# Optimization experiments

Hardware: AMD Instinct MI355X
Metric: run time of the kernel (lower is better)

The kernel has to match this reference:

```python
import jax, jax.numpy as jnp
import numpy as np

D = 256      # d_model
NH = 8       # heads
NL = 3       # layers
DFF = 1024   # ffn hidden
WIN = 64     # attention window
EPS = 1e-5


def _sin_pos_embed(L, d):
    # Sinusoidal positional embedding, matches _create_pos_embedding.
    pos = jnp.arange(L, dtype=jnp.float32)[:, None]
    div = jnp.exp(jnp.arange(0, d, 2, dtype=jnp.float32) * (-np.log(10000.0) / d))
    pe = jnp.zeros((L, d), jnp.float32)
    pe = pe.at[:, 0::2].set(jnp.sin(pos * div))
    pe = pe.at[:, 1::2].set(jnp.cos(pos * div))
    return pe  # [L, D]


def _layer_norm(x, scale, bias):
    m = jnp.mean(x, axis=-1, keepdims=True)
    v = jnp.mean(jnp.square(x - m), axis=-1, keepdims=True)
    return (x - m) * jax.lax.rsqrt(v + EPS) * scale + bias


def _mha(x, Wi, bi, Wo, bo):
    # x: [N, S, D]; Wi: [3D, D]; Wo: [D, D]. torch nn.MultiheadAttention semantics (eval, no dropout).
    N, S, _ = x.shape
    dh = D // NH
    qkv = x @ Wi.T + bi                       # [N, S, 3D]
    q, k, v = jnp.split(qkv, 3, axis=-1)
    q = q.reshape(N, S, NH, dh).transpose(0, 2, 1, 3) * (dh ** -0.5)
    k = k.reshape(N, S, NH, dh).transpose(0, 2, 1, 3)
    v = v.reshape(N, S, NH, dh).transpose(0, 2, 1, 3)
    attn = jax.nn.softmax(jnp.einsum('nhqd,nhkd->nhqk', q, k), axis=-1)
    out = jnp.einsum('nhqk,nhkd->nhqd', attn, v)
    out = out.transpose(0, 2, 1, 3).reshape(N, S, D)
    return out @ Wo.T + bo


def setup_inputs() -> dict:
    key = jax.random.key(0)
    ks = jax.random.split(key, 16)
    s = 0.02
    return {
        'features': jax.random.normal(ks[0], (32, D, 32, 32), jnp.float32),
        'in_proj_w': jax.random.normal(ks[1], (NL, 3 * D, D), jnp.float32) * s,
        'in_proj_b': jnp.zeros((NL, 3 * D), jnp.float32),
        'out_proj_w': jax.random.normal(ks[2], (NL, D, D), jnp.float32) * s,
        'out_proj_b': jnp.zeros((NL, D), jnp.float32),
        'w1': jax.random.normal(ks[3], (NL, DFF, D), jnp.float32) * s,
        'b1': jnp.zeros((NL, DFF), jnp.float32),
        'w2': jax.random.normal(ks[4], (NL, D, DFF), jnp.float32) * s,
        'b2': jnp.zeros((NL, D), jnp.float32),
        'ln1_s': jnp.ones((NL, D), jnp.float32),
        'ln1_b': jnp.zeros((NL, D), jnp.float32),
        'ln2_s': jnp.ones((NL, D), jnp.float32),
        'ln2_b': jnp.zeros((NL, D), jnp.float32),
        'fnorm_s': jnp.ones((D,), jnp.float32),
        'fnorm_b': jnp.zeros((D,), jnp.float32),
    }


def reference(features, in_proj_w, in_proj_b, out_proj_w, out_proj_b,
              w1, b1, w2, b2, ln1_s, ln1_b, ln2_s, ln2_b, fnorm_s, fnorm_b):
    B, C, H, W = features.shape
    L = H * W
    x = features.reshape(B, C, L).transpose(0, 2, 1)   # [B, L, D]
    x = x + _sin_pos_embed(L, D)[None]                 # L == 1024 == max_len, no interp
    nw = L // WIN                                      # non-overlapping windows
    for i in range(NL):
        # windowed self-attention: all windows batched in one MHA call
        xw = x.reshape(B * nw, WIN, D)
        att = _mha(xw, in_proj_w[i], in_proj_b[i], out_proj_w[i], out_proj_b[i])
        att = att.reshape(B, L, D)
        x = _layer_norm(x + att, ln1_s[i], ln1_b[i])
        h = jax.nn.gelu(x @ w1[i].T + b1[i], approximate=False) @ w2[i].T + b2[i]
        x = _layer_norm(x + h, ln2_s[i], ln2_b[i])
    x = _layer_norm(x, fnorm_s, fnorm_b)
    return x.transpose(0, 2, 1).reshape(B, C, H, W)
```

## Files before the change

### kernel.cpp

```cpp
#include <hip/hip_runtime.h>
#include <hip/hip_bf16.h>
#include <hip/hip_fp16.h>

#define BSZ 32
#define DM 256
#define LSEQ 1024
#define MTOK (BSZ * LSEQ)
#define NHEAD 8
#define DHEAD 32
#define WIN 64
#define DFF 1024
#define M8 ((size_t)MTOK * 8)

typedef short bf16x8 __attribute__((ext_vector_type(8)));
typedef float f32x4 __attribute__((ext_vector_type(4)));
typedef unsigned short u16x8 __attribute__((ext_vector_type(8)));
typedef _Float16 f16x4 __attribute__((ext_vector_type(4)));

union BF { __hip_bfloat16 h; unsigned short u; };
__device__ __forceinline__ unsigned short f2bf(float f) { BF b; b.h = __float2bfloat16(f); return b.u; }
__device__ __forceinline__ float bf2f(unsigned short u) { return __uint_as_float((unsigned)u << 16); }

#define GLD_LDS16(gp, lp) __builtin_amdgcn_global_load_lds( \
    (const __attribute__((address_space(1))) void*)(gp),    \
    (__attribute__((address_space(3))) void*)(lp), 16, 0, 0)

__device__ __forceinline__ float gelu_fast(float x) {
    float t = x * (0.7978845608f + 0.0356774081f * x * x);
    return x / (1.0f + __expf(-2.0f * t));
}

__global__ __launch_bounds__(256) void cvt_kernel(
    const float* __restrict__ s, unsigned short* __restrict__ d,
    int N, int K, int nl)
{
    int K8 = K >> 3;
    int per = N * K8;
    int c = blockIdx.x * 256 + threadIdx.x;
    if (c >= per * nl) return;
    int layer = c / per, rem = c - layer * per;
    int n = rem / K8, kc = rem - n * K8;
    const float* sp = s + (size_t)layer * N * K + (size_t)n * K + kc * 8;
    float4 v0 = *(const float4*)sp, v1 = *(const float4*)(sp + 4);
    uint4 o;
    o.x = f2bf(v0.x) | ((unsigned)f2bf(v0.y) << 16);
    o.y = f2bf(v0.z) | ((unsigned)f2bf(v0.w) << 16);
    o.z = f2bf(v1.x) | ((unsigned)f2bf(v1.y) << 16);
    o.w = f2bf(v1.z) | ((unsigned)f2bf(v1.w) << 16);
    *(uint4*)(d + (size_t)layer * N * K + (size_t)kc * N * 8 + (size_t)n * 8) = o;
}

__global__ __launch_bounds__(256) void pe_kernel(float* __restrict__ PE)
{
    int l = blockIdx.x, c = threadIdx.x;
    int i2 = c & ~1;
    float div = expf(-9.210340371976184f * (float)i2 / 256.0f);
    float ang = (float)l * div;
    PE[l * DM + c] = (c & 1) ? cosf(ang) : sinf(ang);
}

__global__ __launch_bounds__(256) void embed_kernel(
    const float* __restrict__ F, const float* __restrict__ PE,
    _Float16* __restrict__ Xh, unsigned short* __restrict__ Xb)
{
    __shared__ float tile[64][65];
    int b = blockIdx.z, l0 = blockIdx.y * 64, c0 = blockIdx.x * 64;
    int tid = threadIdx.x;
    int li = tid & 63, c4 = tid >> 6;
    #pragma unroll
    for (int it = 0; it < 16; ++it) {
        int c = c4 + it * 4;
        tile[c][li] = F[((size_t)(b * DM + c0 + c)) * LSEQ + l0 + li];
    }
    __syncthreads();
    int ci = tid & 63, l4 = tid >> 6;
    #pragma unroll
    for (int it = 0; it < 16; ++it) {
        int l = l4 + it * 4;
        float x = tile[ci][l] + PE[(l0 + l) * DM + c0 + ci];
        Xh[((size_t)b * LSEQ + l0 + l) * DM + c0 + ci] = (_Float16)x;
    }
    int ch = tid >> 5;
    int lx = tid & 31;
    #pragma unroll
    for (int rd = 0; rd < 2; ++rd) {
        int l = lx + rd * 32;
        unsigned short vs[8];
        #pragma unroll
        for (int e = 0; e < 8; ++e) {
            int c = ch * 8 + e;
            vs[e] = f2bf(tile[c][l] + PE[(l0 + l) * DM + c0 + c]);
        }
        uint4 o;
        o.x = vs[0] | ((unsigned)vs[1] << 16);
        o.y = vs[2] | ((unsigned)vs[3] << 16);
        o.z = vs[4] | ((unsigned)vs[5] << 16);
        o.w = vs[6] | ((unsigned)vs[7] << 16);
        *(uint4*)(Xb + ((size_t)((c0 >> 3) + ch)) * M8 +
                  (size_t)(b * LSEQ + l0 + l) * 8) = o;
    }
}

__global__ __launch_bounds__(256) void gemm_mfma_kernel(
    const unsigned short* __restrict__ A, const unsigned short* __restrict__ Bw,
    const float* __restrict__ bias, unsigned short* __restrict__ Cb,
    int M, int N, int K, int gelu)
{
    __shared__ __align__(16) unsigned short Asm[2][4096];
    __shared__ __align__(16) unsigned short Bsm[2][4096];

    const int tid = threadIdx.x;
    const int lane = tid & 63, wave = tid >> 6;
    const int l15 = lane & 15, quad = lane >> 4;
    const int wm = (wave & 1) * 64, wn = (wave >> 1) * 64;

    const int nbx = gridDim.x, nby = gridDim.y;
    const int nwg = nbx * nby;
    int lin = blockIdx.y * nbx + blockIdx.x;
    int logical = lin;
    if ((nwg & 7) == 0) {
        int cpx = nwg >> 3;
        logical = (lin & 7) * cpx + (lin >> 3);
    }
    const int mi = logical / nby;
    const int ni = logical - mi * nby;
    const int m0 = mi * 128, n0 = ni * 128;

    const size_t Ma8 = (size_t)M * 8, Nb8 = (size_t)N * 8;

    auto stage = [&](int buf, int t) {
        const size_t kcb = (size_t)t * 4;
        #pragma unroll
        for (int s = 0; s < 4; ++s) {
            const int u = wave * 4 + s;
            const int kc = (u >> 1) & 3;
            const int h = u & 1;
            if (u < 8) {
                GLD_LDS16(A + (kcb + kc) * Ma8 + (size_t)(m0 + h * 64 + lane) * 8,
                          &Asm[buf][kc * 1024 + h * 512 + lane * 8]);
            } else {
                GLD_LDS16(Bw + (kcb + kc) * Nb8 + (size_t)(n0 + h * 64 + lane) * 8,
                          &Bsm[buf][kc * 1024 + h * 512 + lane * 8]);
            }
        }
    };

    f32x4 acc[4][4] = {};
    const int steps = K >> 5;

    stage(0, 0);
    __syncthreads();

    int cur = 0;
    for (int t = 0; t < steps; ++t) {
        if (t + 1 < steps) stage(cur ^ 1, t + 1);
        const unsigned short* Ab = &Asm[cur][quad * 1024];
        const unsigned short* Bb = &Bsm[cur][quad * 1024];
        bf16x8 av[4], bv[4];
        #pragma unroll
        for (int i = 0; i < 4; ++i)
            av[i] = *(const bf16x8*)(Ab + (wm + i * 16 + l15) * 8);
        #pragma unroll
        for (int j = 0; j < 4; ++j)
            bv[j] = *(const bf16x8*)(Bb + (wn + j * 16 + l15) * 8);
        #pragma unroll
        for (int i = 0; i < 4; ++i)
            #pragma unroll
            for (int j = 0; j < 4; ++j)
                acc[i][j] = __builtin_amdgcn_mfma_f32_16x16x32_bf16(
                    bv[j], av[i], acc[i][j], 0, 0, 0);
        __syncthreads();
        cur ^= 1;
    }

    float4 bb[4];
    #pragma unroll
    for (int j = 0; j < 4; ++j)
        bb[j] = *(const float4*)(bias + n0 + wn + j * 16 + quad * 4);

    #pragma unroll
    for (int i = 0; i < 4; ++i) {
        const size_t m8 = (size_t)(m0 + wm + i * 16 + l15) * 8;
        #pragma unroll
        for (int j = 0; j < 4; ++j) {
            int nb = n0 + wn + j * 16 + quad * 4;
            float v0 = acc[i][j][0] + bb[j].x;
            float v1 = acc[i][j][1] + bb[j].y;
            float v2 = acc[i][j][2] + bb[j].z;
            float v3 = acc[i][j][3] + bb[j].w;
            if (gelu) {
                v0 = gelu_fast(v0); v1 = gelu_fast(v1);
                v2 = gelu_fast(v2); v3 = gelu_fast(v3);
            }
            uint2 o;
            o.x = f2bf(v0) | ((unsigned)f2bf(v1) << 16);
            o.y = f2bf(v2) | ((unsigned)f2bf(v3) << 16);
            *(uint2*)(Cb + ((size_t)(nb >> 3)) * Ma8 + m8 + (nb & 7)) = o;
        }
    }
}

__global__ __launch_bounds__(256) void gemm_ln_kernel(
    const unsigned short* __restrict__ A, const unsigned short* __restrict__ Bw,
    const float* __restrict__ bias, const _Float16* __restrict__ resid,
    const float* __restrict__ lns, const float* __restrict__ lnb,
    _Float16* __restrict__ Xh, unsigned short* __restrict__ Xb, int K)
{
    __shared__ float Ss[256], Sq[256];
    const int tid = threadIdx.x;
    const int lane = tid & 63, wave = tid >> 6;
    const int l15 = lane & 15, quad = lane >> 4;
    const int wn = wave * 64;
    const int m0 = blockIdx.x * 64;
    const size_t Nb8 = (size_t)DM * 8;
    const size_t astep = 4 * M8, bstep = 4 * Nb8;

    const unsigned short* ap[4];
    const unsigned short* bp[4];
    #pragma unroll
    for (int i = 0; i < 4; ++i)
        ap[i] = A + quad * M8 + (size_t)(m0 + i * 16 + l15) * 8;
    #pragma unroll
    for (int j = 0; j < 4; ++j)
        bp[j] = Bw + quad * Nb8 + (size_t)(wn + j * 16 + l15) * 8;

    f32x4 acc[4][4] = {};
    bf16x8 aA[4], bA[4], aB[4], bB[4];
    #pragma unroll
    for (int i = 0; i < 4; ++i) aA[i] = *(const bf16x8*)(ap[i]);
    #pragma unroll
    for (int j = 0; j < 4; ++j) bA[j] = *(const bf16x8*)(bp[j]);

    const int iters = K >> 5;
    for (int t = 0; t < iters; t += 2) {
        size_t o1 = (size_t)(t + 1);
        #pragma unroll
        for (int i = 0; i < 4; ++i) aB[i] = *(const bf16x8*)(ap[i] + o1 * astep);
        #pragma unroll
        for (int j = 0; j < 4; ++j) bB[j] = *(const bf16x8*)(bp[j] + o1 * bstep);
        #pragma unroll
        for (int i = 0; i < 4; ++i)
            #pragma unroll
            for (int j = 0; j < 4; ++j)
                acc[i][j] = __builtin_amdgcn_mfma_f32_16x16x32_bf16(
                    bA[j], aA[i], acc[i][j], 0, 0, 0);
        size_t o2 = (size_t)((t + 2 < iters) ? t + 2 : iters - 1);
        #pragma unroll
        for (int i = 0; i < 4; ++i) aA[i] = *(const bf16x8*)(ap[i] + o2 * astep);
        #pragma unroll
        for (int j = 0; j < 4; ++j) bA[j] = *(const bf16x8*)(bp[j] + o2 * bstep);
        #pragma unroll
        for (int i = 0; i < 4; ++i)
            #pragma unroll
            for (int j = 0; j < 4; ++j)
                acc[i][j] = __builtin_amdgcn_mfma_f32_16x16x32_bf16(
                    bB[j], aB[i], acc[i][j], 0, 0, 0);
    }

    float4 bj[4];
    #pragma unroll
    for (int j = 0; j < 4; ++j)
        bj[j] = *(const float4*)(bias + wn + j * 16 + quad * 4);
    #pragma unroll
    for (int i = 0; i < 4; ++i) {
        const _Float16* rp = resid + (size_t)(m0 + i * 16 + l15) * DM + wn + quad * 4;
        #pragma unroll
        for (int j = 0; j < 4; ++j) {
            f16x4 rr = *(const f16x4*)(rp + j * 16);
            acc[i][j][0] += bj[j].x + (float)rr[0];
            acc[i][j][1] += bj[j].y + (float)rr[1];
            acc[i][j][2] += bj[j].z + (float)rr[2];
            acc[i][j][3] += bj[j].w + (float)rr[3];
        }
    }

    #pragma unroll
    for (int i = 0; i < 4; ++i) {
        float s = 0.f, q = 0.f;
        #pragma unroll
        for (int j = 0; j < 4; ++j)
            #pragma unroll
            for (int r = 0; r < 4; ++r) {
                float x = acc[i][j][r];
                s += x; q = fmaf(x, x, q);
            }
        s += __shfl_xor(s, 16); q += __shfl_xor(q, 16);
        s += __shfl_xor(s, 32); q += __shfl_xor(q, 32);
        if (quad == 0) {
            Ss[wave * 64 + i * 16 + l15] = s;
            Sq[wave * 64 + i * 16 + l15] = q;
        }
    }
    __syncthreads();

    float4 scj[4], bbj[4];
    #pragma unroll
    for (int j = 0; j < 4; ++j) {
        scj[j] = *(const float4*)(lns + wn + j * 16 + quad * 4);
        bbj[j] = *(const float4*)(lnb + wn + j * 16 + quad * 4);
    }
    #pragma unroll
    for (int i = 0; i < 4; ++i) {
        int row = i * 16 + l15;
        float s = Ss[row] + Ss[64 + row] + Ss[128 + row] + Ss[192 + row];
        float q = Sq[row] + Sq[64 + row] + Sq[128 + row] + Sq[192 + row];
        float mean = s * (1.0f / 256.0f);
        float var  = q * (1.0f / 256.0f) - mean * mean;
        float rinv = rsqrtf(var + 1e-5f);
        #pragma unroll
        for (int j = 0; j < 4; ++j) {
            acc[i][j][0] = (acc[i][j][0] - mean) * rinv * scj[j].x + bbj[j].x;
            acc[i][j][1] = (acc[i][j][1] - mean) * rinv * scj[j].y + bbj[j].y;
            acc[i][j][2] = (acc[i][j][2] - mean) * rinv * scj[j].z + bbj[j].z;
            acc[i][j][3] = (acc[i][j][3] - mean) * rinv * scj[j].w + bbj[j].w;
        }
    }

    #pragma unroll
    for (int i = 0; i < 4; ++i) {
        int m = m0 + i * 16 + l15;
        size_t gf = (size_t)m * DM + wn + quad * 4;
        size_t m8 = (size_t)m * 8;
        #pragma unroll
        for (int j = 0; j < 4; ++j) {
            f16x4 oh = { (_Float16)acc[i][j][0], (_Float16)acc[i][j][1],
                         (_Float16)acc[i][j][2], (_Float16)acc[i][j][3] };
            *(f16x4*)(Xh + gf + j * 16) = oh;
            int nb = wn + j * 16 + quad * 4;
            uint2 ob;
            ob.x = f2bf(acc[i][j][0]) | ((unsigned)f2bf(acc[i][j][1]) << 16);
            ob.y = f2bf(acc[i][j][2]) | ((unsigned)f2bf(acc[i][j][3]) << 16);
            *(uint2*)(Xb + ((size_t)(nb >> 3)) * M8 + m8 + (nb & 7)) = ob;
        }
    }
}

__global__ __launch_bounds__(64) void attn_mfma_kernel(
    const unsigned short* __restrict__ QKV, unsigned short* __restrict__ ATT)
{
    __shared__ __align__(16) char smem[22016];
    unsigned short* Qs = (unsigned short*)smem;
    unsigned short* Ks = (unsigned short*)(smem + 4096);
    unsigned short* VT = (unsigned short*)(smem + 8192);
    unsigned short* Ps = (unsigned short*)(smem + 12800);
    float*          Po = (float*)(smem + 12800);

    const int wg = blockIdx.x, h = blockIdx.y;
    const int base = wg * WIN;
    const int lane = threadIdx.x;
    const int l15 = lane & 15, quad = lane >> 4;
    const float scale = 0.17677669529663687f;

    #pragma unroll
    for (int dc = 0; dc < 4; ++dc) {
        GLD_LDS16(QKV + ((size_t)(h * 4 + dc)) * M8 + (size_t)(base + lane) * 8,
                  Qs + dc * 512 + (size_t)lane * 8);
        GLD_LDS16(QKV + ((size_t)(32 + h * 4 + dc)) * M8 + (size_t)(base + lane) * 8,
                  Ks + dc * 512 + (size_t)lane * 8);
    }
    u16x8 vv[4];
    #pragma unroll
    for (int cc = 0; cc < 4; ++cc)
        vv[cc] = *(const u16x8*)(QKV + ((size_t)(64 + h * 4 + cc)) * M8 +
                                 (size_t)(base + lane) * 8);
    #pragma unroll
    for (int cc = 0; cc < 4; ++cc)
        #pragma unroll
        for (int e = 0; e < 8; ++e)
            VT[(cc * 8 + e) * 72 + lane] = vv[cc][e];
    __syncthreads();

    const f32x4 zero4 = {0.f, 0.f, 0.f, 0.f};
    bf16x8 aq[4], bk[4];
    #pragma unroll
    for (int i = 0; i < 4; ++i)
        aq[i] = *(const bf16x8*)(Qs + quad * 512 + (i * 16 + l15) * 8);
    #pragma unroll
    for (int j = 0; j < 4; ++j)
        bk[j] = *(const bf16x8*)(Ks + quad * 512 + (j * 16 + l15) * 8);
    f32x4 S[4][4];
    #pragma unroll
    for (int i = 0; i < 4; ++i)
        #pragma unroll
        for (int j = 0; j < 4; ++j)
            S[i][j] = __builtin_amdgcn_mfma_f32_16x16x32_bf16(aq[i], bk[j], zero4, 0, 0, 0);

    float mx[4][4], sum[4][4];
    #pragma unroll
    for (int i = 0; i < 4; ++i)
        #pragma unroll
        for (int r = 0; r < 4; ++r) {
            float m0 = -1e30f;
            #pragma unroll
            for (int j = 0; j < 4; ++j) {
                S[i][j][r] *= scale;
                m0 = fmaxf(m0, S[i][j][r]);
            }
            mx[i][r] = m0;
        }
    #pragma unroll
    for (int off = 1; off < 16; off <<= 1)
        #pragma unroll
        for (int i = 0; i < 4; ++i)
            #pragma unroll
            for (int r = 0; r < 4; ++r)
                mx[i][r] = fmaxf(mx[i][r], __shfl_xor(mx[i][r], off));
    #pragma unroll
    for (int i = 0; i < 4; ++i)
        #pragma unroll
        for (int r = 0; r < 4; ++r) {
            float s0 = 0.f;
            #pragma unroll
            for (int j = 0; j < 4; ++j) {
                float e = __expf(S[i][j][r] - mx[i][r]);
                S[i][j][r] = e;
                s0 += e;
            }
            sum[i][r] = s0;
        }
    #pragma unroll
    for (int off = 1; off < 16; off <<= 1)
        #pragma unroll
        for (int i = 0; i < 4; ++i)
            #pragma unroll
            for (int r = 0; r < 4; ++r)
                sum[i][r] += __shfl_xor(sum[i][r], off);

    #pragma unroll
    for (int i = 0; i < 4; ++i)
        #pragma unroll
        for (int r = 0; r < 4; ++r) {
            float inv = 1.0f / sum[i][r];
            #pragma unroll
            for (int j = 0; j < 4; ++j)
                Ps[(i * 16 + quad * 4 + r) * 72 + j * 16 + l15] =
                    f2bf(S[i][j][r] * inv);
        }
    asm volatile("s_waitcnt lgkmcnt(0)" ::: "memory");

    bf16x8 ap0[4], ap1[4], bv0[2], bv1[2];
    #pragma unroll
    for (int i = 0; i < 4; ++i) {
        ap0[i] = *(const bf16x8*)(Ps + (i * 16 + l15) * 72 + quad * 8);
        ap1[i] = *(const bf16x8*)(Ps + (i * 16 + l15) * 72 + 32 + quad * 8);
    }
    #pragma unroll
    for (int jd = 0; jd < 2; ++jd) {
        bv0[jd] = *(const bf16x8*)(VT + (jd * 16 + l15) * 72 + quad * 8);
        bv1[jd] = *(const bf16x8*)(VT + (jd * 16 + l15) * 72 + 32 + quad * 8);
    }
    f32x4 O[4][2];
    #pragma unroll
    for (int i = 0; i < 4; ++i)
        #pragma unroll
        for (int jd = 0; jd < 2; ++jd) {
            f32x4 t = __builtin_amdgcn_mfma_f32_16x16x32_bf16(ap0[i], bv0[jd], zero4, 0, 0, 0);
            O[i][jd] = __builtin_amdgcn_mfma_f32_16x16x32_bf16(ap1[i], bv1[jd], t, 0, 0, 0);
        }
    asm volatile("s_waitcnt lgkmcnt(0)" ::: "memory");

    #pragma unroll
    for (int i = 0; i < 4; ++i)
        #pragma unroll
        for (int jd = 0; jd < 2; ++jd)
            #pragma unroll
            for (int r = 0; r < 4; ++r)
                Po[(i * 16 + quad * 4 + r) * 36 + jd * 16 + l15] = O[i][jd][r];
    asm volatile("s_waitcnt lgkmcnt(0)" ::: "memory");

    #pragma unroll
    for (int g = 0; g < 4; ++g) {
        f32x4 t0 = *(const f32x4*)(Po + lane * 36 + g * 8);
        f32x4 t1 = *(const f32x4*)(Po + lane * 36 + g * 8 + 4);
        uint4 w;
        w.x = f2bf(t0[0]) | ((unsigned)f2bf(t0[1]) << 16);
        w.y = f2bf(t0[2]) | ((unsigned)f2bf(t0[3]) << 16);
        w.z = f2bf(t1[0]) | ((unsigned)f2bf(t1[1]) << 16);
        w.w = f2bf(t1[2]) | ((unsigned)f2bf(t1[3]) << 16);
        *(uint4*)(ATT + ((size_t)(h * 4 + g)) * M8 + (size_t)(base + lane) * 8) = w;
    }
}

__global__ __launch_bounds__(256) void out_ln_kernel(
    const _Float16* __restrict__ Xh, const float* __restrict__ sc,
    const float* __restrict__ bi, float* __restrict__ out)
{
    __shared__ float tile[64][257];
    __shared__ float mean_s[64], rinv_s[64];
    int b = blockIdx.y, l0 = blockIdx.x * 64;
    int tid = threadIdx.x, wave = tid >> 6, lane = tid & 63;
    int c = lane * 4;
    #pragma unroll
    for (int it = 0; it < 16; ++it) {
        int tl = wave * 16 + it;
        f16x4 h = *(const f16x4*)(Xh + ((size_t)(b * LSEQ + l0 + tl)) * DM + c);
        float vx = (float)h[0], vy = (float)h[1], vz = (float)h[2], vw = (float)h[3];
        tile[tl][c + 0] = vx; tile[tl][c + 1] = vy;
        tile[tl][c + 2] = vz; tile[tl][c + 3] = vw;
        float sm = vx + vy + vz + vw;
        float sq = vx * vx + vy * vy + vz * vz + vw * vw;
        #pragma unroll
        for (int off = 32; off > 0; off >>= 1) {
            sm += __shfl_down(sm, off);
            sq += __shfl_down(sq, off);
        }
        if (lane == 0) {
            float mean = sm * (1.0f / 256.0f);
            float var  = sq * (1.0f / 256.0f) - mean * mean;
            mean_s[tl] = mean;
            rinv_s[tl] = rsqrtf(var + 1e-5f);
        }
    }
    __syncthreads();
    int lout = tid & 63, crow = tid >> 6;
    #pragma unroll
    for (int ct = 0; ct < 4; ++ct) {
        int c0 = ct * 64;
        #pragma unroll
        for (int it = 0; it < 16; ++it) {
            int cc = c0 + crow + it * 4;
            float v = tile[lout][cc];
            out[((size_t)(b * DM + cc)) * LSEQ + l0 + lout] =
                (v - mean_s[lout]) * rinv_s[lout] * sc[cc] + bi[cc];
        }
    }
}

extern "C" void kernel_launch(void* const* d_in, const int* in_sizes, int n_in,
                              void* d_out, int out_size, void* d_ws, size_t ws_size,
                              hipStream_t stream)
{
    const float* F   = (const float*)d_in[0];
    const float* Wi  = (const float*)d_in[1];
    const float* Bi  = (const float*)d_in[2];
    const float* Wo  = (const float*)d_in[3];
    const float* Bo  = (const float*)d_in[4];
    const float* W1  = (const float*)d_in[5];
    const float* B1  = (const float*)d_in[6];
    const float* W2  = (const float*)d_in[7];
    const float* B2  = (const float*)d_in[8];
    const float* L1s = (const float*)d_in[9];
    const float* L1b = (const float*)d_in[10];
    const float* L2s = (const float*)d_in[11];
    const float* L2b = (const float*)d_in[12];
    const float* Fs  = (const float*)d_in[13];
    const float* Fb  = (const float*)d_in[14];

    char* w = (char*)d_ws;
    _Float16*       Xh   = (_Float16*)w;
    unsigned short* QKVb = (unsigned short*)(w + 33554432);
    unsigned short* Hb   = (unsigned short*)(w + 83886080);
    unsigned short* Xb   = (unsigned short*)(w + 150994944);
    unsigned short* ATTb = (unsigned short*)(w + 167772160);
    unsigned short* WB   = (unsigned short*)(w + 184549376);
    float*          PE   = (float*)(w + 189267968);
    unsigned short* Wib  = WB;
    unsigned short* Wob  = WB + 589824;
    unsigned short* W1b  = WB + 786432;
    unsigned short* W2b  = WB + 1572864;

    cvt_kernel<<<(3 * 768 * 32 + 255) / 256, 256, 0, stream>>>(Wi, Wib, 768, 256, 3);
    cvt_kernel<<<(3 * 256 * 32 + 255) / 256, 256, 0, stream>>>(Wo, Wob, 256, 256, 3);
    cvt_kernel<<<(3 * 1024 * 32 + 255) / 256, 256, 0, stream>>>(W1, W1b, 1024, 256, 3);
    cvt_kernel<<<(3 * 256 * 128 + 255) / 256, 256, 0, stream>>>(W2, W2b, 256, 1024, 3);
    pe_kernel<<<LSEQ, 256, 0, stream>>>(PE);
    embed_kernel<<<dim3(DM / 64, LSEQ / 64, BSZ), 256, 0, stream>>>(F, PE, Xh, Xb);

    for (int i = 0; i < 3; ++i) {
        gemm_mfma_kernel<<<dim3(MTOK / 128, 768 / 128), 256, 0, stream>>>(
            Xb, Wib + (size_t)i * 196608, Bi + i * 768, QKVb, MTOK, 768, DM, 0);
        attn_mfma_kernel<<<dim3(BSZ * (LSEQ / WIN), NHEAD), 64, 0, stream>>>(QKVb, ATTb);
        gemm_ln_kernel<<<MTOK / 64, 256, 0, stream>>>(
            ATTb, Wob + (size_t)i * 65536, Bo + i * DM, Xh,
            L1s + i * DM, L1b + i * DM, Xh, Xb, DM);
        gemm_mfma_kernel<<<dim3(MTOK / 128, DFF / 128), 256, 0, stream>>>(
            Xb, W1b + (size_t)i * 262144, B1 + i * DFF, Hb, MTOK, DFF, DM, 1);
        gemm_ln_kernel<<<MTOK / 64, 256, 0, stream>>>(
            Hb, W2b + (size_t)i * 262144, B2 + i * DM, Xh,
            L2s + i * DM, L2b + i * DM, Xh, Xb, DFF);
    }

    out_ln_kernel<<<dim3(LSEQ / 64, BSZ), 256, 0, stream>>>(
        Xh, Fs, Fb, (float*)d_out);
}
```

Baseline: 551.4 us.

## Stage GEMM-LN operand tiles through double-buffered LDS via async global-to-LDS loads

The fused GEMM+LayerNorm kernel used to load A and B fragments straight from global memory into registers in each wave, so the four waves each refetched the same A rows. It now stages each K-step's A tile (64x32) and B tile (256x32) into double-buffered shared memory with global_load_lds, prefetching the next step while computing the current one, and reads fragments from LDS. This removes redundant A fetches and should give more coalesced loads, at the cost of a block barrier per K-step and about 40KB of LDS, which may limit occupancy.

After: 572.6 us. 1.04x slower.

```diff
diff --git a/kernel.cpp b/kernel.cpp
--- a/kernel.cpp
+++ b/kernel.cpp
@@ -206,6 +206,8 @@
     const float* __restrict__ lns, const float* __restrict__ lnb,
     _Float16* __restrict__ Xh, unsigned short* __restrict__ Xb, int K)
 {
+    __shared__ __align__(16) unsigned short Asm[2][2048];
+    __shared__ __align__(16) unsigned short Bsm[2][8192];
     __shared__ float Ss[256], Sq[256];
     const int tid = threadIdx.x;
     const int lane = tid & 63, wave = tid >> 6;
@@ -213,48 +215,50 @@
     const int wn = wave * 64;
     const int m0 = blockIdx.x * 64;
     const size_t Nb8 = (size_t)DM * 8;
-    const size_t astep = 4 * M8, bstep = 4 * Nb8;
-
-    const unsigned short* ap[4];
-    const unsigned short* bp[4];
-    #pragma unroll
-    for (int i = 0; i < 4; ++i)
-        ap[i] = A + quad * M8 + (size_t)(m0 + i * 16 + l15) * 8;
-    #pragma unroll
-    for (int j = 0; j < 4; ++j)
-        bp[j] = Bw + quad * Nb8 + (size_t)(wn + j * 16 + l15) * 8;
+
+    auto stage = [&](int buf, int t) {
+        const size_t kcb = (size_t)t * 4;
+        #pragma unroll
+        for (int s = 0; s < 5; ++s) {
+            const int u = wave * 5 + s;
+            if (u < 4) {
+                GLD_LDS16(A + (kcb + u) * M8 + (size_t)(m0 + lane) * 8,
+                          &Asm[buf][u * 512 + lane * 8]);
+            } else {
+                const int v = u - 4;
+                const int kc = v >> 2, q = v & 3;
+                GLD_LDS16(Bw + (kcb + kc) * Nb8 + (size_t)(q * 64 + lane) * 8,
+                          &Bsm[buf][kc * 2048 + q * 512 + lane * 8]);
+            }
+        }
+    };
 
     f32x4 acc[4][4] = {};
-    bf16x8 aA[4], bA[4], aB[4], bB[4];
-    #pragma unroll
-    for (int i = 0; i < 4; ++i) aA[i] = *(const bf16x8*)(ap[i]);
-    #pragma unroll
-    for (int j = 0; j < 4; ++j) bA[j] = *(const bf16x8*)(bp[j]);
-
-    const int iters = K >> 5;
-    for (int t = 0; t < iters; t += 2) {
-        size_t o1 = (size_t)(t + 1);
-        #pragma unroll
-        for (int i = 0; i < 4; ++i) aB[i] = *(const bf16x8*)(ap[i] + o1 * astep);
-        #pragma unroll
-        for (int j = 0; j < 4; ++j) bB[j] = *(const bf16x8*)(bp[j] + o1 * bstep);
+    const int steps = K >> 5;
+
+    stage(0, 0);
+    __syncthreads();
+
+    int cur = 0;
+    for (int t = 0; t < steps; ++t) {
+        if (t + 1 < steps) stage(cur ^ 1, t + 1);
+        const unsigned short* Ab = &Asm[cur][quad * 512];
+        const unsigned short* Bb = &Bsm[cur][quad * 2048];
+        bf16x8 av[4], bv[4];
+        #pragma unroll
+        for (int i = 0; i < 4; ++i)
+            av[i] = *(const bf16x8*)(Ab + (i * 16 + l15) * 8);
+        #pragma unroll
+        for (int j = 0; j < 4; ++j)
+            bv[j] = *(const bf16x8*)(Bb + (wn + j * 16 + l15) * 8);
         #pragma unroll
         for (int i = 0; i < 4; ++i)
             #pragma unroll
             for (int j = 0; j < 4; ++j)
                 acc[i][j] = __builtin_amdgcn_mfma_f32_16x16x32_bf16(
-                    bA[j], aA[i], acc[i][j], 0, 0, 0);
-        size_t o2 = (size_t)((t + 2 < iters) ? t + 2 : iters - 1);
-        #pragma unroll
-        for (int i = 0; i < 4; ++i) aA[i] = *(const bf16x8*)(ap[i] + o2 * astep);
-        #pragma unroll
-        for (int j = 0; j < 4; ++j) bA[j] = *(const bf16x8*)(bp[j] + o2 * bstep);
-        #pragma unroll
-        for (int i = 0; i < 4; ++i)
-            #pragma unroll
-            for (int j = 0; j < 4; ++j)
-                acc[i][j] = __builtin_amdgcn_mfma_f32_16x16x32_bf16(
-                    bB[j], aB[i], acc[i][j], 0, 0, 0);
+                    bv[j], av[i], acc[i][j], 0, 0, 0);
+        __syncthreads();
+        cur ^= 1;
     }
 
     float4 bj[4];
```
